# Kernel optimization log

Measured on AMD Instinct MI355X. Metric: run time of the kernel, lower is better.

Reference implementation:

```python
import jax, jax.numpy as jnp
import numpy as np

EMBED = 1024
HEAD = 64
SEQ = 2048
BATCH = 8


def setup_inputs() -> dict:
    key = jax.random.key(0)
    kx, kq, kk, kv = jax.random.split(key, 4)
    x = jax.random.normal(kx, (BATCH, SEQ, EMBED), dtype=jnp.float32)
    # torch nn.Linear weight is [out,in]; we store [in,out] so y = x @ W
    Wq = jax.random.normal(kq, (EMBED, HEAD), dtype=jnp.float32) * (EMBED ** -0.5)
    Wk = jax.random.normal(kk, (EMBED, HEAD), dtype=jnp.float32) * (EMBED ** -0.5)
    Wv = jax.random.normal(kv, (EMBED, HEAD), dtype=jnp.float32) * (EMBED ** -0.5)
    return {"x": x, "Wq": Wq, "Wk": Wk, "Wv": Wv}


def reference(x, Wq, Wk, Wv):
    # x: [B,T,C]; single-head causal attention. Scale uses C (embedding dim),
    # matching the original module's C ** (-0.5). Dropout in eval mode (identity).
    B, T, C = x.shape
    q = x @ Wq  # [B,T,H]
    k = x @ Wk  # [B,T,H]
    v = x @ Wv  # [B,T,H]
    scores = jnp.einsum('bqh,bkh->bqk', q, k) * (C ** -0.5)  # [B,T,T]
    causal = jnp.tril(jnp.ones((T, T), dtype=bool))
    scores = jnp.where(causal, scores, -jnp.inf)
    weights = jax.nn.softmax(scores, axis=-1)
    return jnp.einsum('bqk,bkh->bqh', weights, v)  # [B,T,H]
```

## Files before the change

kernel.cpp:

```cpp
#include <hip/hip_runtime.h>
#include <hip/hip_bf16.h>
#include <math.h>

#define BATCH 8
#define SEQ 2048
#define EMBED 1024
#define HEAD 64
#define NROWS (BATCH*SEQ)

typedef short bf16x8 __attribute__((ext_vector_type(8)));
typedef short bf16x4 __attribute__((ext_vector_type(4)));
typedef float f32x4  __attribute__((ext_vector_type(4)));

__device__ inline short f2bf(float f) {
    __hip_bfloat16 h = __float2bfloat16(f);
    return *(short*)&h;
}
__device__ inline float bf2f(short s) {
    __hip_bfloat16 h = *(__hip_bfloat16*)&s;
    return __bfloat162float(h);
}

#define NSLOT 144
__device__ __host__ inline int triOff(int qt) {
    int g = qt >> 2;
    return 2 * g * (g + 1) + (qt & 3) * (g + 1);
}

__global__ __launch_bounds__(256) void prep_w(
    const float* __restrict__ Wq, const float* __restrict__ Wk,
    const float* __restrict__ Wv, short* __restrict__ wt)
{
    int g    = blockIdx.x * 256 + threadIdx.x;
    int lane = g & 63;
    int frag = g >> 6;
    int k32  = frag & 31;
    int ct   = frag >> 5;
    int col  = ct * 16 + (lane & 15);
    int mm   = col >> 6, cc = col & 63;
    const float* W = (mm == 0) ? Wq : ((mm == 1) ? Wk : Wv);
    int kb = k32 * 32 + (lane >> 4) * 8;
    bf16x8 o;
#pragma unroll
    for (int j = 0; j < 8; j++)
        o[j] = f2bf(W[(size_t)(kb + j) * HEAD + cc]);
    *(bf16x8*)&wt[(size_t)g * 8] = o;
}

__global__ __launch_bounds__(512, 4) void proj_kernel(
    const float* __restrict__ x, const short* __restrict__ wt,
    short* __restrict__ q, short* __restrict__ k, short* __restrict__ vt)
{
    __shared__ short xs[32][1024];
    float* psum = (float*)&xs[0][0];

    const int tid  = threadIdx.x;
    const int wave = tid >> 6, lane = tid & 63;
    const int m16  = lane & 15, quad = lane >> 4;
    const int cg   = wave & 3;
    const int kh   = wave >> 2;
    const int r0   = blockIdx.x * 32;

    {
        const int row  = tid >> 4;
        const int col4 = tid & 15;
        const float* xr = x + (size_t)(r0 + row) * EMBED;
#pragma unroll
        for (int h = 0; h < 2; h++) {
            float4 f[8];
#pragma unroll
            for (int i = 0; i < 8; i++)
                f[i] = *(const float4*)&xr[(h * 8 + i) * 64 + col4 * 4];
#pragma unroll
            for (int i = 0; i < 8; i++) {
                int c  = (h * 8 + i) * 64 + col4 * 4;
                int k8 = c >> 3, rem = c & 7;
                int cs = ((k8 ^ (row & 7)) << 3) + rem;
                bf16x4 bv;
                bv[0] = f2bf(f[i].x); bv[1] = f2bf(f[i].y);
                bv[2] = f2bf(f[i].z); bv[3] = f2bf(f[i].w);
                *(bf16x4*)&xs[row][cs] = bv;
            }
        }
    }
    __syncthreads();

    f32x4 acc[2][3];
#pragma unroll
    for (int mt = 0; mt < 2; mt++)
#pragma unroll
        for (int j = 0; j < 3; j++) acc[mt][j] = (f32x4){0.f, 0.f, 0.f, 0.f};

#pragma unroll 4
    for (int s = 0; s < 16; s++) {
        int k32  = kh * 16 + s;
        int ksw  = ((k32 * 4 + quad) ^ (m16 & 7)) << 3;
        bf16x8 a0 = *(const bf16x8*)&xs[m16][ksw];
        bf16x8 a1 = *(const bf16x8*)&xs[16 + m16][ksw];
#pragma unroll
        for (int j = 0; j < 3; j++) {
            int ct = cg * 3 + j;
            bf16x8 bb = *(const bf16x8*)&wt[(size_t)((ct * 32 + k32) * 64 + lane) * 8];
            acc[0][j] = __builtin_amdgcn_mfma_f32_16x16x32_bf16(a0, bb, acc[0][j], 0, 0, 0);
            acc[1][j] = __builtin_amdgcn_mfma_f32_16x16x32_bf16(a1, bb, acc[1][j], 0, 0, 0);
        }
    }

    __syncthreads();
    if (kh == 1) {
        float* p = psum + ((size_t)(cg * 64 + lane) * 24);
#pragma unroll
        for (int mt = 0; mt < 2; mt++)
#pragma unroll
            for (int j = 0; j < 3; j++)
                *(f32x4*)&p[(mt * 3 + j) * 4] = acc[mt][j];
    }
    __syncthreads();
    if (kh == 0) {
        const float* p = psum + ((size_t)(cg * 64 + lane) * 24);
        const int bb = r0 >> 11;
        const int tb = r0 & 2047;
#pragma unroll
        for (int mt = 0; mt < 2; mt++)
#pragma unroll
            for (int j = 0; j < 3; j++) {
                f32x4 o = acc[mt][j] + *(const f32x4*)&p[(mt * 3 + j) * 4];
                int gcol = (cg * 3 + j) * 16 + m16;
                int mm = gcol >> 6, cc = gcol & 63;
                if (mm < 2) {
                    short* op = (mm == 0) ? q : k;
#pragma unroll
                    for (int reg = 0; reg < 4; reg++) {
                        int row = r0 + mt * 16 + quad * 4 + reg;
                        op[(size_t)row * HEAD + cc] = f2bf(o[reg]);
                    }
                } else {
                    bf16x4 pk;
                    pk[0] = f2bf(o[0]); pk[1] = f2bf(o[1]);
                    pk[2] = f2bf(o[2]); pk[3] = f2bf(o[3]);
                    int t = tb + mt * 16 + quad * 4;
                    *(bf16x4*)&vt[(((size_t)bb * 64 + cc) << 11) + t] = pk;
                }
            }
    }
}

__global__ __launch_bounds__(256, 5) void attn_kernel(
    const short* __restrict__ qg, const short* __restrict__ kg,
    const short* __restrict__ vtg,
    short* __restrict__ pO, float* __restrict__ pl)
{
    __shared__ short ksh[64][72];
    __shared__ short vsh[64][72];
    __shared__ short psh[4][16][72];

    const int qt  = blockIdx.x;
    const int seg = blockIdx.y;
    const int b   = blockIdx.z;
    const int c0  = seg * 4;
    const int c1  = min(seg * 4 + 4, qt + 1);
    if (c0 >= c1) return;

    const int tid  = threadIdx.x;
    const int wave = tid >> 6, lane = tid & 63;
    const int m16  = lane & 15, quad = lane >> 4;
    const float scale = 0.03125f;

    const short* qb  = qg  + (size_t)b * SEQ * HEAD;
    const short* kb  = kg  + (size_t)b * SEQ * HEAD;
    const short* vtb = vtg + (size_t)b * HEAD * SEQ;

    bf16x8 a_q0, a_q1;
    {
        const int qrow = qt * 64 + wave * 16 + m16;
        a_q0 = *(const bf16x8*)&qb[(size_t)qrow * HEAD + quad * 8];
        a_q1 = *(const bf16x8*)&qb[(size_t)qrow * HEAD + 32 + quad * 8];
    }
    const int myrow = qt * 64 + wave * 16 + m16;

    f32x4 o_acc[4];
#pragma unroll
    for (int i = 0; i < 4; i++) o_acc[i] = (f32x4){0.f, 0.f, 0.f, 0.f};
    float lsum = 0.f;

    const int srow = tid >> 3;
    const int sc8  = (tid & 7) * 8;

    bf16x8 kr0 = *(const bf16x8*)&kb[(size_t)(c0 * 64 + srow) * HEAD + sc8];
    bf16x8 kr1 = *(const bf16x8*)&kb[(size_t)(c0 * 64 + 32 + srow) * HEAD + sc8];
    bf16x8 vr0 = *(const bf16x8*)&vtb[((size_t)srow << 11) + c0 * 64 + sc8];
    bf16x8 vr1 = *(const bf16x8*)&vtb[((size_t)(srow + 32) << 11) + c0 * 64 + sc8];

    for (int c = c0; c < c1; c++) {
        const int t0 = c * 64;
        __syncthreads();
        *(bf16x8*)&ksh[srow][sc8]      = kr0;
        *(bf16x8*)&ksh[srow + 32][sc8] = kr1;
        *(bf16x8*)&vsh[srow][sc8]      = vr0;
        *(bf16x8*)&vsh[srow + 32][sc8] = vr1;
        __syncthreads();
        if (c + 1 < c1) {
            const int tn = (c + 1) * 64;
            kr0 = *(const bf16x8*)&kb[(size_t)(tn + srow) * HEAD + sc8];
            kr1 = *(const bf16x8*)&kb[(size_t)(tn + 32 + srow) * HEAD + sc8];
            vr0 = *(const bf16x8*)&vtb[((size_t)srow << 11) + tn + sc8];
            vr1 = *(const bf16x8*)&vtb[((size_t)(srow + 32) << 11) + tn + sc8];
        }

        f32x4 s_t[4];
#pragma unroll
        for (int nt = 0; nt < 4; nt++) {
            bf16x8 ak0 = *(const bf16x8*)&ksh[nt * 16 + m16][quad * 8];
            bf16x8 ak1 = *(const bf16x8*)&ksh[nt * 16 + m16][32 + quad * 8];
            f32x4 acc = (f32x4){0.f, 0.f, 0.f, 0.f};
            acc = __builtin_amdgcn_mfma_f32_16x16x32_bf16(ak0, a_q0, acc, 0, 0, 0);
            acc = __builtin_amdgcn_mfma_f32_16x16x32_bf16(ak1, a_q1, acc, 0, 0, 0);
            s_t[nt] = acc;
        }

        if (c == qt) {
#pragma unroll
            for (int nt = 0; nt < 4; nt++) {
                bf16x4 pk;
#pragma unroll
                for (int r = 0; r < 4; r++) {
                    int tt = t0 + nt * 16 + quad * 4 + r;
                    float p = (tt <= myrow) ? __expf(s_t[nt][r] * scale) : 0.f;
                    lsum += p;
                    pk[r] = f2bf(p);
                }
                *(bf16x4*)&psh[wave][m16][nt * 16 + quad * 4] = pk;
            }
        } else {
#pragma unroll
            for (int nt = 0; nt < 4; nt++) {
                bf16x4 pk;
#pragma unroll
                for (int r = 0; r < 4; r++) {
                    float p = __expf(s_t[nt][r] * scale);
                    lsum += p;
                    pk[r] = f2bf(p);
                }
                *(bf16x4*)&psh[wave][m16][nt * 16 + quad * 4] = pk;
            }
        }

#pragma unroll
        for (int ss = 0; ss < 2; ss++) {
            bf16x8 a_p = *(const bf16x8*)&psh[wave][m16][ss * 32 + quad * 8];
#pragma unroll
            for (int ht = 0; ht < 4; ht++) {
                bf16x8 b_v = *(const bf16x8*)&vsh[ht * 16 + m16][ss * 32 + quad * 8];
                o_acc[ht] = __builtin_amdgcn_mfma_f32_16x16x32_bf16(a_p, b_v, o_acc[ht], 0, 0, 0);
            }
        }
    }

    lsum += __shfl_xor(lsum, 16, 64);
    lsum += __shfl_xor(lsum, 32, 64);
    const size_t slot  = (size_t)b * NSLOT + triOff(qt) + seg;
    const size_t pbase = slot * 64;
#pragma unroll
    for (int ht = 0; ht < 4; ht++) {
#pragma unroll
        for (int r = 0; r < 4; r++) {
            int rowt = wave * 16 + quad * 4 + r;
            pO[(pbase + rowt) * 64 + ht * 16 + m16] = f2bf(o_acc[ht][r]);
        }
    }
    if (quad == 0) {
        pl[pbase + wave * 16 + m16] = lsum;
    }
}

__global__ __launch_bounds__(256) void combine_kernel(
    const short* __restrict__ pO, const float* __restrict__ pl,
    float* __restrict__ out)
{
    int g   = blockIdx.x * 256 + threadIdx.x;
    int h8  = (g & 7) * 8;
    int row = (g >> 3) & 2047;
    int b   = g >> 14;
    int qt  = row >> 6, lr = row & 63;
    int ns  = (qt >> 2) + 1;
    size_t base = (size_t)b * NSLOT + triOff(qt);
    float O[8] = {0.f, 0.f, 0.f, 0.f, 0.f, 0.f, 0.f, 0.f};
    float L = 0.f;
    for (int s = 0; s < ns; s++) {
        bf16x8 ov = *(const bf16x8*)&pO[((base + s) * 64 + lr) * 64 + h8];
#pragma unroll
        for (int j = 0; j < 8; j++) O[j] += bf2f(ov[j]);
        L += pl[(base + s) * 64 + lr];
    }
    float inv = 1.f / L;
    float4 o0 = {O[0] * inv, O[1] * inv, O[2] * inv, O[3] * inv};
    float4 o1 = {O[4] * inv, O[5] * inv, O[6] * inv, O[7] * inv};
    *(float4*)&out[(size_t)g * 8]     = o0;
    *(float4*)&out[(size_t)g * 8 + 4] = o1;
}

extern "C" void kernel_launch(void* const* d_in, const int* in_sizes, int n_in,
                              void* d_out, int out_size, void* d_ws, size_t ws_size,
                              hipStream_t stream) {
    const float* x  = (const float*)d_in[0];
    const float* Wq = (const float*)d_in[1];
    const float* Wk = (const float*)d_in[2];
    const float* Wv = (const float*)d_in[3];
    float* out = (float*)d_out;

    short* q  = (short*)d_ws;
    short* k  = q + (size_t)NROWS * HEAD;
    short* vt = k + (size_t)NROWS * HEAD;
    short* wt = vt + (size_t)NROWS * HEAD;
    short* pO = wt + 196608;
    float* pl = (float*)(pO + (size_t)BATCH * NSLOT * 64 * 64);

    prep_w<<<96, 256, 0, stream>>>(Wq, Wk, Wv, wt);
    proj_kernel<<<512, 512, 0, stream>>>(x, wt, q, k, vt);
    attn_kernel<<<dim3(32, 8, 8), 256, 0, stream>>>(q, k, vt, pO, pl);
    combine_kernel<<<512, 256, 0, stream>>>(pO, pl, out);
}
```

Measured before the change: 126.3 us.

## Pair adjacent query tiles per block to share K/V LDS tiles

Each attention block now runs 8 waves covering two consecutive 64-row query tiles, and all of them share one K/V chunk staged in shared memory. Waves of the lower tile skip the chunk beyond their causal limit but still reach every barrier. The aim is to halve global K/V traffic and staging work per query tile, and to spread each staging load across twice as many threads. In exchange, blocks are larger with fewer per CU, and the lower tile's waves sit idle during the extra diagonal chunk, which makes load balance coarser.

```diff
diff --git a/kernel.cpp b/kernel.cpp
--- a/kernel.cpp
+++ b/kernel.cpp
@@ -145,25 +145,29 @@
     }
 }
 
-__global__ __launch_bounds__(256, 5) void attn_kernel(
+__global__ __launch_bounds__(512, 4) void attn_kernel(
     const short* __restrict__ qg, const short* __restrict__ kg,
     const short* __restrict__ vtg,
     short* __restrict__ pO, float* __restrict__ pl)
 {
     __shared__ short ksh[64][72];
     __shared__ short vsh[64][72];
-    __shared__ short psh[4][16][72];
-
-    const int qt  = blockIdx.x;
+    __shared__ short psh[8][16][72];
+
+    const int pr  = blockIdx.x;
     const int seg = blockIdx.y;
     const int b   = blockIdx.z;
+    const int qt_hi = pr * 2 + 1;
     const int c0  = seg * 4;
-    const int c1  = min(seg * 4 + 4, qt + 1);
+    const int c1  = min(seg * 4 + 4, qt_hi + 1);
     if (c0 >= c1) return;
 
     const int tid  = threadIdx.x;
     const int wave = tid >> 6, lane = tid & 63;
     const int m16  = lane & 15, quad = lane >> 4;
+    const int qsel = wave >> 2;
+    const int w4   = wave & 3;
+    const int qt   = pr * 2 + qsel;
     const float scale = 0.03125f;
 
     const short* qb  = qg  + (size_t)b * SEQ * HEAD;
@@ -171,12 +175,11 @@
     const short* vtb = vtg + (size_t)b * HEAD * SEQ;
 
     bf16x8 a_q0, a_q1;
+    const int myrow = qt * 64 + w4 * 16 + m16;
     {
-        const int qrow = qt * 64 + wave * 16 + m16;
-        a_q0 = *(const bf16x8*)&qb[(size_t)qrow * HEAD + quad * 8];
-        a_q1 = *(const bf16x8*)&qb[(size_t)qrow * HEAD + 32 + quad * 8];
-    }
-    const int myrow = qt * 64 + wave * 16 + m16;
+        a_q0 = *(const bf16x8*)&qb[(size_t)myrow * HEAD + quad * 8];
+        a_q1 = *(const bf16x8*)&qb[(size_t)myrow * HEAD + 32 + quad * 8];
+    }
 
     f32x4 o_acc[4];
 #pragma unroll
@@ -186,72 +189,68 @@
     const int srow = tid >> 3;
     const int sc8  = (tid & 7) * 8;
 
-    bf16x8 kr0 = *(const bf16x8*)&kb[(size_t)(c0 * 64 + srow) * HEAD + sc8];
-    bf16x8 kr1 = *(const bf16x8*)&kb[(size_t)(c0 * 64 + 32 + srow) * HEAD + sc8];
-    bf16x8 vr0 = *(const bf16x8*)&vtb[((size_t)srow << 11) + c0 * 64 + sc8];
-    bf16x8 vr1 = *(const bf16x8*)&vtb[((size_t)(srow + 32) << 11) + c0 * 64 + sc8];
+    bf16x8 kr = *(const bf16x8*)&kb[(size_t)(c0 * 64 + srow) * HEAD + sc8];
+    bf16x8 vr = *(const bf16x8*)&vtb[((size_t)srow << 11) + c0 * 64 + sc8];
 
     for (int c = c0; c < c1; c++) {
         const int t0 = c * 64;
         __syncthreads();
-        *(bf16x8*)&ksh[srow][sc8]      = kr0;
-        *(bf16x8*)&ksh[srow + 32][sc8] = kr1;
-        *(bf16x8*)&vsh[srow][sc8]      = vr0;
-        *(bf16x8*)&vsh[srow + 32][sc8] = vr1;
+        *(bf16x8*)&ksh[srow][sc8] = kr;
+        *(bf16x8*)&vsh[srow][sc8] = vr;
         __syncthreads();
         if (c + 1 < c1) {
             const int tn = (c + 1) * 64;
-            kr0 = *(const bf16x8*)&kb[(size_t)(tn + srow) * HEAD + sc8];
-            kr1 = *(const bf16x8*)&kb[(size_t)(tn + 32 + srow) * HEAD + sc8];
-            vr0 = *(const bf16x8*)&vtb[((size_t)srow << 11) + tn + sc8];
-            vr1 = *(const bf16x8*)&vtb[((size_t)(srow + 32) << 11) + tn + sc8];
-        }
-
-        f32x4 s_t[4];
-#pragma unroll
-        for (int nt = 0; nt < 4; nt++) {
-            bf16x8 ak0 = *(const bf16x8*)&ksh[nt * 16 + m16][quad * 8];
-            bf16x8 ak1 = *(const bf16x8*)&ksh[nt * 16 + m16][32 + quad * 8];
-            f32x4 acc = (f32x4){0.f, 0.f, 0.f, 0.f};
-            acc = __builtin_amdgcn_mfma_f32_16x16x32_bf16(ak0, a_q0, acc, 0, 0, 0);
-            acc = __builtin_amdgcn_mfma_f32_16x16x32_bf16(ak1, a_q1, acc, 0, 0, 0);
-            s_t[nt] = acc;
-        }
-
-        if (c == qt) {
+            kr = *(const bf16x8*)&kb[(size_t)(tn + srow) * HEAD + sc8];
+            vr = *(const bf16x8*)&vtb[((size_t)srow << 11) + tn + sc8];
+        }
+
+        if (c <= qt) {
+            f32x4 s_t[4];
 #pragma unroll
             for (int nt = 0; nt < 4; nt++) {
-                bf16x4 pk;
-#pragma unroll
-                for (int r = 0; r < 4; r++) {
-                    int tt = t0 + nt * 16 + quad * 4 + r;
-                    float p = (tt <= myrow) ? __expf(s_t[nt][r] * scale) : 0.f;
-                    lsum += p;
-                    pk[r] = f2bf(p);
+                bf16x8 ak0 = *(const bf16x8*)&ksh[nt * 16 + m16][quad * 8];
+                bf16x8 ak1 = *(const bf16x8*)&ksh[nt * 16 + m16][32 + quad * 8];
+                f32x4 acc = (f32x4){0.f, 0.f, 0.f, 0.f};
+                acc = __builtin_amdgcn_mfma_f32_16x16x32_bf16(ak0, a_q0, acc, 0, 0, 0);
+                acc = __builtin_amdgcn_mfma_f32_16x16x32_bf16(ak1, a_q1, acc, 0, 0, 0);
+                s_t[nt] = acc;
+            }
+
+            if (c == qt) {
+#pragma unroll
+                for (int nt = 0; nt < 4; nt++) {
+                    bf16x4 pk;
+#pragma unroll
+                    for (int r = 0; r < 4; r++) {
+                        int tt = t0 + nt * 16 + quad * 4 + r;
+                        float p = (tt <= myrow) ? __expf(s_t[nt][r] * scale) : 0.f;
+                        lsum += p;
+                        pk[r] = f2bf(p);
+                    }
+                    *(bf16x4*)&psh[wave][m16][nt * 16 + quad * 4] = pk;
                 }
-                *(bf16x4*)&psh[wave][m16][nt * 16 + quad * 4] = pk;
-            }
-        } else {
-#pragma unroll
-            for (int nt = 0; nt < 4; nt++) {
-                bf16x4 pk;
-#pragma unroll
-                for (int r = 0; r < 4; r++) {
-                    float p = __expf(s_t[nt][r] * scale);
-                    lsum += p;
-                    pk[r] = f2bf(p);
+            } else {
+#pragma unroll
+                for (int nt = 0; nt < 4; nt++) {
+                    bf16x4 pk;
+#pragma unroll
+                    for (int r = 0; r < 4; r++) {
+                        float p = __expf(s_t[nt][r] * scale);
+                        lsum += p;
+                        pk[r] = f2bf(p);
+                    }
+                    *(bf16x4*)&psh[wave][m16][nt * 16 + quad * 4] = pk;
                 }
-                *(bf16x4*)&psh[wave][m16][nt * 16 + quad * 4] = pk;
-            }
-        }
-
-#pragma unroll
-        for (int ss = 0; ss < 2; ss++) {
-            bf16x8 a_p = *(const bf16x8*)&psh[wave][m16][ss * 32 + quad * 8];
-#pragma unroll
-            for (int ht = 0; ht < 4; ht++) {
-                bf16x8 b_v = *(const bf16x8*)&vsh[ht * 16 + m16][ss * 32 + quad * 8];
-                o_acc[ht] = __builtin_amdgcn_mfma_f32_16x16x32_bf16(a_p, b_v, o_acc[ht], 0, 0, 0);
+            }
+
+#pragma unroll
+            for (int ss = 0; ss < 2; ss++) {
+                bf16x8 a_p = *(const bf16x8*)&psh[wave][m16][ss * 32 + quad * 8];
+#pragma unroll
+                for (int ht = 0; ht < 4; ht++) {
+                    bf16x8 b_v = *(const bf16x8*)&vsh[ht * 16 + m16][ss * 32 + quad * 8];
+                    o_acc[ht] = __builtin_amdgcn_mfma_f32_16x16x32_bf16(a_p, b_v, o_acc[ht], 0, 0, 0);
+                }
             }
         }
     }
@@ -264,12 +263,12 @@
     for (int ht = 0; ht < 4; ht++) {
 #pragma unroll
         for (int r = 0; r < 4; r++) {
-            int rowt = wave * 16 + quad * 4 + r;
+            int rowt = w4 * 16 + quad * 4 + r;
             pO[(pbase + rowt) * 64 + ht * 16 + m16] = f2bf(o_acc[ht][r]);
         }
     }
     if (quad == 0) {
-        pl[pbase + wave * 16 + m16] = lsum;
+        pl[pbase + w4 * 16 + m16] = lsum;
     }
 }
 
@@ -317,6 +316,6 @@
 
     prep_w<<<96, 256, 0, stream>>>(Wq, Wk, Wv, wt);
     proj_kernel<<<512, 512, 0, stream>>>(x, wt, q, k, vt);
-    attn_kernel<<<dim3(32, 8, 8), 256, 0, stream>>>(q, k, vt, pO, pl);
+    attn_kernel<<<dim3(16, 8, 8), 512, 0, stream>>>(q, k, vt, pO, pl);
     combine_kernel<<<512, 256, 0, stream>>>(pO, pl, out);
 }
```

Result: no change. 127.9 us (+1.3%).

## Replace split-K attention plus combine kernel with two-group in-block reduction

Applied to the files above, without the earlier changes.

The attention kernel previously split each query tile's keys into segments of four chunks across blocks, wrote bf16 partial outputs and sums to workspace, and ran a separate combine kernel. It now uses 512-thread blocks per query tile in which two 4-wave groups process alternating key chunks, then reduce through shared memory and write the normalized fp32 output directly. This removes the partial-result traffic and the extra kernel launch. The cost is fewer, more unbalanced blocks: only 256 blocks, and long causal rows for late query tiles are now handled by a single block.

```diff
diff --git a/kernel.cpp b/kernel.cpp
--- a/kernel.cpp
+++ b/kernel.cpp
@@ -19,12 +19,6 @@
 __device__ inline float bf2f(short s) {
     __hip_bfloat16 h = *(__hip_bfloat16*)&s;
     return __bfloat162float(h);
-}
-
-#define NSLOT 144
-__device__ __host__ inline int triOff(int qt) {
-    int g = qt >> 2;
-    return 2 * g * (g + 1) + (qt & 3) * (g + 1);
 }
 
 __global__ __launch_bounds__(256) void prep_w(
@@ -145,73 +139,80 @@
     }
 }
 
-__global__ __launch_bounds__(256, 5) void attn_kernel(
+__global__ __launch_bounds__(512, 2) void attn_kernel(
     const short* __restrict__ qg, const short* __restrict__ kg,
-    const short* __restrict__ vtg,
-    short* __restrict__ pO, float* __restrict__ pl)
+    const short* __restrict__ vtg, float* __restrict__ out)
 {
-    __shared__ short ksh[64][72];
-    __shared__ short vsh[64][72];
-    __shared__ short psh[4][16][72];
-
-    const int qt  = blockIdx.x;
-    const int seg = blockIdx.y;
-    const int b   = blockIdx.z;
-    const int c0  = seg * 4;
-    const int c1  = min(seg * 4 + 4, qt + 1);
-    if (c0 >= c1) return;
+    __shared__ short ksh[2][64][72];
+    __shared__ short vsh[2][64][72];
+    __shared__ short psh[8][16][72];
+
+    const int qt = blockIdx.x;
+    const int b  = blockIdx.y;
 
     const int tid  = threadIdx.x;
     const int wave = tid >> 6, lane = tid & 63;
     const int m16  = lane & 15, quad = lane >> 4;
+    const int g    = wave >> 2;
+    const int w4   = wave & 3;
     const float scale = 0.03125f;
 
     const short* qb  = qg  + (size_t)b * SEQ * HEAD;
     const short* kb  = kg  + (size_t)b * SEQ * HEAD;
     const short* vtb = vtg + (size_t)b * HEAD * SEQ;
 
-    bf16x8 a_q0, a_q1;
-    {
-        const int qrow = qt * 64 + wave * 16 + m16;
-        a_q0 = *(const bf16x8*)&qb[(size_t)qrow * HEAD + quad * 8];
-        a_q1 = *(const bf16x8*)&qb[(size_t)qrow * HEAD + 32 + quad * 8];
-    }
-    const int myrow = qt * 64 + wave * 16 + m16;
+    const int myrow = qt * 64 + w4 * 16 + m16;
+    bf16x8 a_q0 = *(const bf16x8*)&qb[(size_t)myrow * HEAD + quad * 8];
+    bf16x8 a_q1 = *(const bf16x8*)&qb[(size_t)myrow * HEAD + 32 + quad * 8];
 
     f32x4 o_acc[4];
 #pragma unroll
     for (int i = 0; i < 4; i++) o_acc[i] = (f32x4){0.f, 0.f, 0.f, 0.f};
     float lsum = 0.f;
 
-    const int srow = tid >> 3;
-    const int sc8  = (tid & 7) * 8;
-
-    bf16x8 kr0 = *(const bf16x8*)&kb[(size_t)(c0 * 64 + srow) * HEAD + sc8];
-    bf16x8 kr1 = *(const bf16x8*)&kb[(size_t)(c0 * 64 + 32 + srow) * HEAD + sc8];
-    bf16x8 vr0 = *(const bf16x8*)&vtb[((size_t)srow << 11) + c0 * 64 + sc8];
-    bf16x8 vr1 = *(const bf16x8*)&vtb[((size_t)(srow + 32) << 11) + c0 * 64 + sc8];
-
-    for (int c = c0; c < c1; c++) {
+    const int gtid = tid & 255;
+    const int srow = gtid >> 3;
+    const int sc8  = (gtid & 7) * 8;
+
+    bf16x8 kr0, kr1, vr0, vr1;
+    if (g <= qt) {
+        const int t0 = g * 64;
+        kr0 = *(const bf16x8*)&kb[(size_t)(t0 + srow) * HEAD + sc8];
+        kr1 = *(const bf16x8*)&kb[(size_t)(t0 + 32 + srow) * HEAD + sc8];
+        vr0 = *(const bf16x8*)&vtb[((size_t)srow << 11) + t0 + sc8];
+        vr1 = *(const bf16x8*)&vtb[((size_t)(srow + 32) << 11) + t0 + sc8];
+    }
+
+    const int R = (qt >> 1) + 1;
+    for (int r = 0; r < R; r++) {
+        const int c      = 2 * r + g;
+        const int active = (c <= qt);
+        __syncthreads();
+        if (active) {
+            *(bf16x8*)&ksh[g][srow][sc8]      = kr0;
+            *(bf16x8*)&ksh[g][srow + 32][sc8] = kr1;
+            *(bf16x8*)&vsh[g][srow][sc8]      = vr0;
+            *(bf16x8*)&vsh[g][srow + 32][sc8] = vr1;
+        }
+        __syncthreads();
+        {
+            const int cn = 2 * (r + 1) + g;
+            if (cn <= qt) {
+                const int tn = cn * 64;
+                kr0 = *(const bf16x8*)&kb[(size_t)(tn + srow) * HEAD + sc8];
+                kr1 = *(const bf16x8*)&kb[(size_t)(tn + 32 + srow) * HEAD + sc8];
+                vr0 = *(const bf16x8*)&vtb[((size_t)srow << 11) + tn + sc8];
+                vr1 = *(const bf16x8*)&vtb[((size_t)(srow + 32) << 11) + tn + sc8];
+            }
+        }
+        if (!active) continue;
+
         const int t0 = c * 64;
-        __syncthreads();
-        *(bf16x8*)&ksh[srow][sc8]      = kr0;
-        *(bf16x8*)&ksh[srow + 32][sc8] = kr1;
-        *(bf16x8*)&vsh[srow][sc8]      = vr0;
-        *(bf16x8*)&vsh[srow + 32][sc8] = vr1;
-        __syncthreads();
-        if (c + 1 < c1) {
-            const int tn = (c + 1) * 64;
-            kr0 = *(const bf16x8*)&kb[(size_t)(tn + srow) * HEAD + sc8];
-            kr1 = *(const bf16x8*)&kb[(size_t)(tn + 32 + srow) * HEAD + sc8];
-            vr0 = *(const bf16x8*)&vtb[((size_t)srow << 11) + tn + sc8];
-            vr1 = *(const bf16x8*)&vtb[((size_t)(srow + 32) << 11) + tn + sc8];
-        }
-
         f32x4 s_t[4];
 #pragma unroll
         for (int nt = 0; nt < 4; nt++) {
-            bf16x8 ak0 = *(const bf16x8*)&ksh[nt * 16 + m16][quad * 8];
-            bf16x8 ak1 = *(const bf16x8*)&ksh[nt * 16 + m16][32 + quad * 8];
+            bf16x8 ak0 = *(const bf16x8*)&ksh[g][nt * 16 + m16][quad * 8];
+            bf16x8 ak1 = *(const bf16x8*)&ksh[g][nt * 16 + m16][32 + quad * 8];
             f32x4 acc = (f32x4){0.f, 0.f, 0.f, 0.f};
             acc = __builtin_amdgcn_mfma_f32_16x16x32_bf16(ak0, a_q0, acc, 0, 0, 0);
             acc = __builtin_amdgcn_mfma_f32_16x16x32_bf16(ak1, a_q1, acc, 0, 0, 0);
@@ -223,11 +224,11 @@
             for (int nt = 0; nt < 4; nt++) {
                 bf16x4 pk;
 #pragma unroll
-                for (int r = 0; r < 4; r++) {
-                    int tt = t0 + nt * 16 + quad * 4 + r;
-                    float p = (tt <= myrow) ? __expf(s_t[nt][r] * scale) : 0.f;
+                for (int rr = 0; rr < 4; rr++) {
+                    int tt = t0 + nt * 16 + quad * 4 + rr;
+                    float p = (tt <= myrow) ? __expf(s_t[nt][rr] * scale) : 0.f;
                     lsum += p;
-                    pk[r] = f2bf(p);
+                    pk[rr] = f2bf(p);
                 }
                 *(bf16x4*)&psh[wave][m16][nt * 16 + quad * 4] = pk;
             }
@@ -236,10 +237,10 @@
             for (int nt = 0; nt < 4; nt++) {
                 bf16x4 pk;
 #pragma unroll
-                for (int r = 0; r < 4; r++) {
-                    float p = __expf(s_t[nt][r] * scale);
+                for (int rr = 0; rr < 4; rr++) {
+                    float p = __expf(s_t[nt][rr] * scale);
                     lsum += p;
-                    pk[r] = f2bf(p);
+                    pk[rr] = f2bf(p);
                 }
                 *(bf16x4*)&psh[wave][m16][nt * 16 + quad * 4] = pk;
             }
@@ -250,7 +251,7 @@
             bf16x8 a_p = *(const bf16x8*)&psh[wave][m16][ss * 32 + quad * 8];
 #pragma unroll
             for (int ht = 0; ht < 4; ht++) {
-                bf16x8 b_v = *(const bf16x8*)&vsh[ht * 16 + m16][ss * 32 + quad * 8];
+                bf16x8 b_v = *(const bf16x8*)&vsh[g][ht * 16 + m16][ss * 32 + quad * 8];
                 o_acc[ht] = __builtin_amdgcn_mfma_f32_16x16x32_bf16(a_p, b_v, o_acc[ht], 0, 0, 0);
             }
         }
@@ -258,45 +259,36 @@
 
     lsum += __shfl_xor(lsum, 16, 64);
     lsum += __shfl_xor(lsum, 32, 64);
-    const size_t slot  = (size_t)b * NSLOT + triOff(qt) + seg;
-    const size_t pbase = slot * 64;
-#pragma unroll
-    for (int ht = 0; ht < 4; ht++) {
-#pragma unroll
-        for (int r = 0; r < 4; r++) {
-            int rowt = wave * 16 + quad * 4 + r;
-            pO[(pbase + rowt) * 64 + ht * 16 + m16] = f2bf(o_acc[ht][r]);
-        }
-    }
-    if (quad == 0) {
-        pl[pbase + wave * 16 + m16] = lsum;
-    }
-}
-
-__global__ __launch_bounds__(256) void combine_kernel(
-    const short* __restrict__ pO, const float* __restrict__ pl,
-    float* __restrict__ out)
-{
-    int g   = blockIdx.x * 256 + threadIdx.x;
-    int h8  = (g & 7) * 8;
-    int row = (g >> 3) & 2047;
-    int b   = g >> 14;
-    int qt  = row >> 6, lr = row & 63;
-    int ns  = (qt >> 2) + 1;
-    size_t base = (size_t)b * NSLOT + triOff(qt);
-    float O[8] = {0.f, 0.f, 0.f, 0.f, 0.f, 0.f, 0.f, 0.f};
-    float L = 0.f;
-    for (int s = 0; s < ns; s++) {
-        bf16x8 ov = *(const bf16x8*)&pO[((base + s) * 64 + lr) * 64 + h8];
-#pragma unroll
-        for (int j = 0; j < 8; j++) O[j] += bf2f(ov[j]);
-        L += pl[(base + s) * 64 + lr];
-    }
-    float inv = 1.f / L;
-    float4 o0 = {O[0] * inv, O[1] * inv, O[2] * inv, O[3] * inv};
-    float4 o1 = {O[4] * inv, O[5] * inv, O[6] * inv, O[7] * inv};
-    *(float4*)&out[(size_t)g * 8]     = o0;
-    *(float4*)&out[(size_t)g * 8 + 4] = o1;
+
+    float* osh  = (float*)&ksh[0][0][0];
+    float* lshA = (float*)&vsh[0][0][0];
+    float* lshB = lshA + 64;
+
+    __syncthreads();
+    if (g == 1) {
+#pragma unroll
+        for (int ht = 0; ht < 4; ht++)
+#pragma unroll
+            for (int rr = 0; rr < 4; rr++)
+                osh[(w4 * 16 + quad * 4 + rr) * 65 + ht * 16 + m16] = o_acc[ht][rr];
+        if (quad == 0) lshB[w4 * 16 + m16] = lsum;
+    } else {
+        if (quad == 0) lshA[w4 * 16 + m16] = lsum;
+    }
+    __syncthreads();
+    if (g == 0) {
+        float* ob = out + ((size_t)b * SEQ + qt * 64) * HEAD;
+#pragma unroll
+        for (int rr = 0; rr < 4; rr++) {
+            const int row = w4 * 16 + quad * 4 + rr;
+            const float inv = 1.f / (lshA[row] + lshB[row]);
+#pragma unroll
+            for (int ht = 0; ht < 4; ht++) {
+                float v = (o_acc[ht][rr] + osh[row * 65 + ht * 16 + m16]) * inv;
+                ob[(size_t)row * HEAD + ht * 16 + m16] = v;
+            }
+        }
+    }
 }
 
 extern "C" void kernel_launch(void* const* d_in, const int* in_sizes, int n_in,
@@ -312,11 +304,8 @@
     short* k  = q + (size_t)NROWS * HEAD;
     short* vt = k + (size_t)NROWS * HEAD;
     short* wt = vt + (size_t)NROWS * HEAD;
-    short* pO = wt + 196608;
-    float* pl = (float*)(pO + (size_t)BATCH * NSLOT * 64 * 64);
 
     prep_w<<<96, 256, 0, stream>>>(Wq, Wk, Wv, wt);
     proj_kernel<<<512, 512, 0, stream>>>(x, wt, q, k, vt);
-    attn_kernel<<<dim3(32, 8, 8), 256, 0, stream>>>(q, k, vt, pO, pl);
-    combine_kernel<<<512, 256, 0, stream>>>(pO, pl, out);
-}
+    attn_kernel<<<dim3(32, 8), 512, 0, stream>>>(q, k, vt, out);
+}
```

Measured after the change: 128.5 us. About the same (+1.8%).
